# Kernel optimization log

Measured on AMD Instinct MI355X. Metric: run time of the kernel, lower is better.

The kernel has to match this reference:

```python
import jax, jax.numpy as jnp
import numpy as np

KH = KW = 3
SH = SW = 1
DH = DW = 1

def _same_padding(ih, iw):
    eff_kh = (KH - 1) * DH + 1
    eff_kw = (KW - 1) * DW + 1
    out_h = (ih + SH - 1) // SH
    out_w = (iw + SW - 1) // SW
    pad_h = max((out_h - 1) * SH + eff_kh - ih, 0)
    pad_w = max((out_w - 1) * SW + eff_kw - iw, 0)
    pad_top = pad_h // 2
    pad_bottom = pad_h - pad_top
    pad_left = pad_w // 2
    pad_right = pad_w - pad_left
    return (pad_top, pad_bottom), (pad_left, pad_right)


def setup_inputs() -> dict:
    key = jax.random.key(0)
    k1, k2, k3 = jax.random.split(key, 3)
    N, C, H, Wd = 32, 192, 56, 56
    Cout = 384
    x = jax.random.normal(k1, (N, C, H, Wd), dtype=jnp.float32)
    # linear weight (Cout, C*KH*KW) with unfold ordering (c, kh, kw) -> OIHW kernel
    W = jax.random.normal(k2, (Cout, C, KH, KW), dtype=jnp.float32) * (1.0 / np.sqrt(C * KH * KW))
    b = jax.random.normal(k3, (Cout,), dtype=jnp.float32) * 0.01
    return {"x": x, "W": W, "b": b}


def reference(x, W, b):
    # ConvLayer: F.pad('same') -> nn.Unfold -> Linear -> reshape, which is
    # mathematically a 2D conv with OIHW kernel W (unfold orders features as c,kh,kw).
    _, _, H, Wd = x.shape
    pad_hw = _same_padding(H, Wd)
    out = jax.lax.conv_general_dilated(
        x, W,
        window_strides=(SH, SW),
        padding=pad_hw,
        rhs_dilation=(DH, DW),
        dimension_numbers=("NCHW", "OIHW", "NCHW"),
    )
    return out + b[None, :, None, None]
```

## Files before the change

### kernel.cpp

```cpp
#include <hip/hip_runtime.h>
#include <cstdint>
#include <cstddef>

#define N_IMG 32
#define C_IN 192
#define HW 56
#define SPAT 3136
#define C_OUT 384
#define HP 58
#define KPOS 9
#define KTOT 1728
#define NSUB 54

#define BM 128
#define BN 256
#define NT_CO 3
#define NT_S  392
#define GRID_MAIN (NT_CO*NT_S)

typedef __attribute__((ext_vector_type(8))) short short8;
typedef __attribute__((ext_vector_type(4))) float f32x4;

__device__ __forceinline__ unsigned short f2bf(float f) {
  union { float f; unsigned u; } v; v.f = f;
  unsigned u = v.u;
  unsigned r = (u + 0x7FFFu + ((u >> 16) & 1u)) >> 16;
  return (unsigned short)r;
}

__device__ __forceinline__ void async_load16(const void* gsrc, void* ldst) {
  __builtin_amdgcn_global_load_lds(
      (const __attribute__((address_space(1))) unsigned int*)gsrc,
      (__attribute__((address_space(3))) unsigned int*)ldst,
      16, 0, 0);
}

__global__ void pack_w(const float* __restrict__ W, unsigned short* __restrict__ Wp) {
  int idx = blockIdx.x*256 + threadIdx.x;
  if (idx >= C_OUT*KPOS*C_IN) return;
  int c   = idx % C_IN;
  int pos = (idx / C_IN) % KPOS;
  int co  = idx / (C_IN*KPOS);
  float v = W[((size_t)co*C_IN + c)*KPOS + pos];
  Wp[idx] = f2bf(v);
}

__global__ void zero_border(unsigned short* __restrict__ Xp) {
  int idx = blockIdx.x*256 + threadIdx.x;
  if (idx >= N_IMG*228*C_IN) return;
  int c    = idx % C_IN;
  int cell = (idx / C_IN) % 228;
  int n    = idx / (C_IN*228);
  int hh, ww;
  if (cell < 116) { hh = (cell < 58) ? 0 : 57; ww = cell % 58; }
  else { int b2 = cell - 116; ww = (b2 < 56) ? 0 : 57; hh = 1 + (b2 % 56); }
  Xp[(((size_t)n*HP + hh)*HP + ww)*C_IN + c] = 0;
}

__global__ void pack_x(const float* __restrict__ x, unsigned short* __restrict__ Xp) {
  __shared__ float tile[64*57];
  int b  = blockIdx.x;
  int cb = b % 3;
  int h  = (b/3) % HW;
  int n  = b / (3*HW);
  int tid = threadIdx.x;
  const float* src = x + (size_t)n*C_IN*SPAT + (size_t)cb*64*SPAT + h*HW;
  #pragma unroll
  for (int i = 0; i < 14; ++i) {
    int idx = i*256 + tid;
    int c = idx / HW, w = idx % HW;
    tile[c*57 + w] = src[(size_t)c*SPAT + w];
  }
  __syncthreads();
  unsigned short* dst = Xp + (((size_t)n*HP + h + 1)*HP + 1)*C_IN + cb*64;
  #pragma unroll
  for (int i = 0; i < 14; ++i) {
    int idx = i*256 + tid;
    int w = idx / 64, c = idx % 64;
    dst[(size_t)w*C_IN + c] = f2bf(tile[c*57 + w]);
  }
}

__global__ __launch_bounds__(512, 2) void conv_gemm(
    const unsigned short* __restrict__ Wp,
    const unsigned short* __restrict__ Xp,
    const float* __restrict__ bias,
    float* __restrict__ out)
{
  __shared__ __attribute__((aligned(16))) unsigned short lds[4][12288];

  int bid = blockIdx.x;
  int wg = (bid & 7) * (GRID_MAIN/8) + (bid >> 3);
  int cotile = wg % NT_CO;
  int stile  = wg / NT_CO;

  const int tid   = threadIdx.x;
  const int lane  = tid & 63;
  const int wv    = tid >> 6;
  const int wm    = wv >> 2;
  const int wn    = wv & 3;
  const int lanep = lane & 15;
  const int laneq = lane >> 4;
  const int l2    = lane >> 2;
  const int l4    = lane & 3;
  const int chunkSw = l4 ^ (l2 & 3);

  const int aRow = cotile*BM + wv*16 + l2;
  const unsigned short* aSrc = Wp + (size_t)aRow*KTOT + chunkSw*8;

  const unsigned short* bSrc0;
  const unsigned short* bSrc1;
  {
    int r0 = (wv*2 + 0)*16 + l2;
    int f0 = stile*BN + r0;
    int n0 = f0 / SPAT, sp0 = f0 % SPAT;
    bSrc0 = Xp + (((size_t)n0*HP + sp0/HW)*HP + sp0%HW)*C_IN + chunkSw*8;
    int r1 = (wv*2 + 1)*16 + l2;
    int f1 = stile*BN + r1;
    int n1 = f1 / SPAT, sp1 = f1 % SPAT;
    bSrc1 = Xp + (((size_t)n1*HP + sp1/HW)*HP + sp1%HW)*C_IN + chunkSw*8;
  }

  unsigned short* aDst  = &lds[0][wv*512];
  unsigned short* bDst0 = &lds[0][4096 + (wv*2 + 0)*512];
  unsigned short* bDst1 = &lds[0][4096 + (wv*2 + 1)*512];

  const int swz8   = (laneq ^ (lanep & 3)) << 3;
  const int aRdBase = (wm*64 + lanep)*32 + swz8;
  const int bRdBase = 4096 + (wn*64 + lanep)*32 + swz8;

  f32x4 acc[4][4];
  #pragma unroll
  for (int mf = 0; mf < 4; ++mf)
    #pragma unroll
    for (int nf = 0; nf < 4; ++nf)
      acc[mf][nf] = (f32x4){0.f, 0.f, 0.f, 0.f};

  auto bOffOf = [](int t) {
    int kh = t / 18;
    int r  = t - kh*18;
    int kw = r / 6;
    int c6 = r - kw*6;
    return (kh*HP + kw)*C_IN + c6*32;
  };

  auto stage = [&](int t) {
    int slot = t & 3;
    async_load16(aSrc + t*32, aDst + slot*12288);
    int bo = bOffOf(t);
    async_load16(bSrc0 + bo, bDst0 + slot*12288);
    async_load16(bSrc1 + bo, bDst1 + slot*12288);
  };

#define PHASE(sv, VMC, DO_STAGE)                                            \
  {                                                                         \
    asm volatile("s_waitcnt vmcnt(" #VMC ")" ::: "memory");                 \
    __builtin_amdgcn_s_barrier();                                           \
    __builtin_amdgcn_sched_barrier(0);                                      \
    const int slot_ = (sv) & 3;                                             \
    const unsigned short* la_ = &lds[slot_][0];                             \
    short8 av_[4], bv_[4];                                                  \
    _Pragma("unroll")                                                       \
    for (int mf = 0; mf < 4; ++mf)                                          \
      av_[mf] = *(const short8*)&la_[aRdBase + mf*512];                     \
    _Pragma("unroll")                                                       \
    for (int nf = 0; nf < 4; ++nf)                                          \
      bv_[nf] = *(const short8*)&la_[bRdBase + nf*512];                     \
    if (DO_STAGE) stage((sv) + 3);                                          \
    __builtin_amdgcn_s_setprio(1);                                          \
    _Pragma("unroll")                                                       \
    for (int mf = 0; mf < 4; ++mf)                                          \
      _Pragma("unroll")                                                     \
      for (int nf = 0; nf < 4; ++nf)                                        \
        acc[mf][nf] = __builtin_amdgcn_mfma_f32_16x16x32_bf16(              \
            av_[mf], bv_[nf], acc[mf][nf], 0, 0, 0);                        \
    __builtin_amdgcn_s_setprio(0);                                          \
    __builtin_amdgcn_sched_barrier(0);                                      \
  }

  stage(0); stage(1); stage(2);

  for (int s = 0; s < 51; ++s)
    PHASE(s, 6, true);
  PHASE(51, 6, false);
  PHASE(52, 3, false);
  PHASE(53, 0, false);
#undef PHASE

  const int coB = cotile*BM + wm*64;
  const int fB  = stile*BN + wn*64;
  #pragma unroll
  for (int nf = 0; nf < 4; ++nf) {
    int f  = fB + nf*16 + lanep;
    int n  = f / SPAT;
    int sp = f % SPAT;
    float* obase = out + (size_t)n*C_OUT*SPAT + sp;
    #pragma unroll
    for (int mf = 0; mf < 4; ++mf) {
      #pragma unroll
      for (int i = 0; i < 4; ++i) {
        int co = coB + mf*16 + laneq*4 + i;
        obase[(size_t)co*SPAT] = acc[mf][nf][i] + bias[co];
      }
    }
  }
}

__global__ void conv_naive(const float* __restrict__ x, const float* __restrict__ W,
                           const float* __restrict__ bias, float* __restrict__ out) {
  size_t idx = (size_t)blockIdx.x*256 + threadIdx.x;
  if (idx >= (size_t)N_IMG*C_OUT*SPAT) return;
  int s  = idx % SPAT;
  int co = (int)((idx / SPAT) % C_OUT);
  int n  = (int)(idx / ((size_t)SPAT*C_OUT));
  int h = s / HW, w = s % HW;
  float acc = bias[co];
  for (int c = 0; c < C_IN; ++c)
    for (int kh = 0; kh < 3; ++kh) {
      int hh = h + kh - 1;
      if (hh < 0 || hh >= HW) continue;
      for (int kw = 0; kw < 3; ++kw) {
        int ww = w + kw - 1;
        if (ww < 0 || ww >= HW) continue;
        acc += x[(((size_t)n*C_IN + c)*HW + hh)*HW + ww]
             * W[(((size_t)co*C_IN + c)*3 + kh)*3 + kw];
      }
    }
  out[idx] = acc;
}

extern "C" void kernel_launch(void* const* d_in, const int* in_sizes, int n_in,
                              void* d_out, int out_size, void* d_ws, size_t ws_size,
                              hipStream_t stream) {
  const float* x = (const float*)d_in[0];
  const float* W = (const float*)d_in[1];
  const float* b = (const float*)d_in[2];
  float* out = (float*)d_out;

  const size_t WP_ELEMS = (size_t)C_OUT*KPOS*C_IN;
  const size_t XP_ELEMS = (size_t)N_IMG*HP*HP*C_IN;
  const size_t NEED = (WP_ELEMS + XP_ELEMS)*2;

  if (ws_size >= NEED) {
    unsigned short* Wp = (unsigned short*)d_ws;
    unsigned short* Xp = Wp + WP_ELEMS;
    zero_border<<<(N_IMG*228*C_IN + 255)/256, 256, 0, stream>>>(Xp);
    pack_w<<<(int)((WP_ELEMS + 255)/256), 256, 0, stream>>>(W, Wp);
    pack_x<<<N_IMG*HW*3, 256, 0, stream>>>(x, Xp);
    conv_gemm<<<GRID_MAIN, 512, 0, stream>>>(Wp, Xp, b, out);
  } else {
    size_t total = (size_t)N_IMG*C_OUT*SPAT;
    conv_naive<<<(int)((total + 255)/256), 256, 0, stream>>>(x, W, b, out);
  }
}
```

Baseline: 186.4 us.

## Double K-depth per stage with triple-buffered LDS and split barrier phases

Raises the K step per pipeline stage from 32 to 64 bf16 channels, halving the number of stages, and switches from a 4-slot ring to 3 fixed LDS buffers of 48KB each. Each stage is consumed in two MFMA half-phases with an XOR-swizzled 8-chunk layout. The barrier and vmcnt waits move to the end of each phase so LDS reads overlap with issuing the next global loads. The aim is to cut barrier and wait overhead per unit of MFMA work. The cost is more LDS per block (144KB), which may limit occupancy below the launch-bounds target of 2 blocks per CU.

Result: slower. 190.3 us (+2.1%).

```diff
diff --git a/kernel.cpp b/kernel.cpp
--- a/kernel.cpp
+++ b/kernel.cpp
@@ -10,7 +10,7 @@
 #define HP 58
 #define KPOS 9
 #define KTOT 1728
-#define NSUB 54
+#define NT 27
 
 #define BM 128
 #define BN 256
@@ -18,6 +18,9 @@
 #define NT_S  392
 #define GRID_MAIN (NT_CO*NT_S)
 
+#define BUF_EL 24576
+#define B_BASE 8192
+
 typedef __attribute__((ext_vector_type(8))) short short8;
 typedef __attribute__((ext_vector_type(4))) float f32x4;
 
@@ -34,6 +37,9 @@
       (__attribute__((address_space(3))) unsigned int*)ldst,
       16, 0, 0);
 }
+
+__device__ __forceinline__ void vm6() { asm volatile("s_waitcnt vmcnt(6)" ::: "memory"); }
+__device__ __forceinline__ void vm0() { asm volatile("s_waitcnt vmcnt(0)" ::: "memory"); }
 
 __global__ void pack_w(const float* __restrict__ W, unsigned short* __restrict__ Wp) {
   int idx = blockIdx.x*256 + threadIdx.x;
@@ -87,7 +93,7 @@
     const float* __restrict__ bias,
     float* __restrict__ out)
 {
-  __shared__ __attribute__((aligned(16))) unsigned short lds[4][12288];
+  __shared__ __attribute__((aligned(16))) unsigned short lds[3][BUF_EL];
 
   int bid = blockIdx.x;
   int wg = (bid & 7) * (GRID_MAIN/8) + (bid >> 3);
@@ -101,33 +107,37 @@
   const int wn    = wv & 3;
   const int lanep = lane & 15;
   const int laneq = lane >> 4;
-  const int l2    = lane >> 2;
-  const int l4    = lane & 3;
-  const int chunkSw = l4 ^ (l2 & 3);
-
-  const int aRow = cotile*BM + wv*16 + l2;
-  const unsigned short* aSrc = Wp + (size_t)aRow*KTOT + chunkSw*8;
-
-  const unsigned short* bSrc0;
-  const unsigned short* bSrc1;
+  const int l3    = lane >> 3;
+  const int l7    = lane & 7;
+  const int gsl   = (l7 ^ l3) << 3;
+
+  const unsigned short* aSrc0;
+  const unsigned short* aSrc1;
   {
-    int r0 = (wv*2 + 0)*16 + l2;
-    int f0 = stile*BN + r0;
-    int n0 = f0 / SPAT, sp0 = f0 % SPAT;
-    bSrc0 = Xp + (((size_t)n0*HP + sp0/HW)*HP + sp0%HW)*C_IN + chunkSw*8;
-    int r1 = (wv*2 + 1)*16 + l2;
-    int f1 = stile*BN + r1;
-    int n1 = f1 / SPAT, sp1 = f1 % SPAT;
-    bSrc1 = Xp + (((size_t)n1*HP + sp1/HW)*HP + sp1%HW)*C_IN + chunkSw*8;
-  }
-
-  unsigned short* aDst  = &lds[0][wv*512];
-  unsigned short* bDst0 = &lds[0][4096 + (wv*2 + 0)*512];
-  unsigned short* bDst1 = &lds[0][4096 + (wv*2 + 1)*512];
-
-  const int swz8   = (laneq ^ (lanep & 3)) << 3;
-  const int aRdBase = (wm*64 + lanep)*32 + swz8;
-  const int bRdBase = 4096 + (wn*64 + lanep)*32 + swz8;
+    int r0 = (0*8 + wv)*8 + l3;
+    aSrc0 = Wp + (size_t)(cotile*BM + r0)*KTOT + gsl;
+    int r1 = (1*8 + wv)*8 + l3;
+    aSrc1 = Wp + (size_t)(cotile*BM + r1)*KTOT + gsl;
+  }
+  const int aOff0 = (0*8 + wv)*512;
+  const int aOff1 = (1*8 + wv)*512;
+
+  const unsigned short* bSrc[4];
+  int bOff[4];
+  #pragma unroll
+  for (int i = 0; i < 4; ++i) {
+    int cbk = i*8 + wv;
+    int rb  = cbk*8 + l3;
+    int f   = stile*BN + rb;
+    int n   = f / SPAT, sp = f % SPAT;
+    bSrc[i] = Xp + (((size_t)n*HP + sp/HW)*HP + sp%HW)*C_IN + gsl;
+    bOff[i] = B_BASE + cbk*512;
+  }
+
+  const int swz = (laneq ^ l7) << 3;
+  const int aRd = (wm*64 + lanep)*64 + ((laneq ^ (lanep & 7)) << 3);
+  const int bRd = B_BASE + (wn*64 + lanep)*64 + ((laneq ^ (lanep & 7)) << 3);
+  (void)swz;
 
   f32x4 acc[4][4];
   #pragma unroll
@@ -137,36 +147,37 @@
       acc[mf][nf] = (f32x4){0.f, 0.f, 0.f, 0.f};
 
   auto bOffOf = [](int t) {
-    int kh = t / 18;
-    int r  = t - kh*18;
-    int kw = r / 6;
-    int c6 = r - kw*6;
-    return (kh*HP + kw)*C_IN + c6*32;
+    int pos = t / 3;
+    int c0  = (t - pos*3) * 64;
+    int kh  = pos / 3, kw = pos - kh*3;
+    return (kh*HP + kw)*C_IN + c0;
   };
 
-  auto stage = [&](int t) {
-    int slot = t & 3;
-    async_load16(aSrc + t*32, aDst + slot*12288);
-    int bo = bOffOf(t);
-    async_load16(bSrc0 + bo, bDst0 + slot*12288);
-    async_load16(bSrc1 + bo, bDst1 + slot*12288);
+  auto stage = [&](int t, unsigned short* base) {
+    const int koff = t*64;
+    async_load16(aSrc0 + koff, base + aOff0);
+    async_load16(aSrc1 + koff, base + aOff1);
+    const int bo = bOffOf(t);
+    #pragma unroll
+    for (int i = 0; i < 4; ++i)
+      async_load16(bSrc[i] + bo, base + bOff[i]);
   };
 
-#define PHASE(sv, VMC, DO_STAGE)                                            \
+#define PHASE(LB, KK, STAGE_STMT, VM_STMT)                                  \
   {                                                                         \
-    asm volatile("s_waitcnt vmcnt(" #VMC ")" ::: "memory");                 \
-    __builtin_amdgcn_s_barrier();                                           \
-    __builtin_amdgcn_sched_barrier(0);                                      \
-    const int slot_ = (sv) & 3;                                             \
-    const unsigned short* la_ = &lds[slot_][0];                             \
+    const unsigned short* lb_ = (LB);                                       \
     short8 av_[4], bv_[4];                                                  \
     _Pragma("unroll")                                                       \
     for (int mf = 0; mf < 4; ++mf)                                          \
-      av_[mf] = *(const short8*)&la_[aRdBase + mf*512];                     \
+      av_[mf] = *(const short8*)&lb_[(aRd + mf*1024) ^ ((KK)*32)];          \
     _Pragma("unroll")                                                       \
     for (int nf = 0; nf < 4; ++nf)                                          \
-      bv_[nf] = *(const short8*)&la_[bRdBase + nf*512];                     \
-    if (DO_STAGE) stage((sv) + 3);                                          \
+      bv_[nf] = *(const short8*)&lb_[(bRd + nf*1024) ^ ((KK)*32)];          \
+    STAGE_STMT;                                                             \
+    __builtin_amdgcn_sched_barrier(0);                                      \
+    __builtin_amdgcn_s_barrier();                                           \
+    asm volatile("s_waitcnt lgkmcnt(0)" ::: "memory");                      \
+    __builtin_amdgcn_sched_barrier(0);                                      \
     __builtin_amdgcn_s_setprio(1);                                          \
     _Pragma("unroll")                                                       \
     for (int mf = 0; mf < 4; ++mf)                                          \
@@ -176,15 +187,27 @@
             av_[mf], bv_[nf], acc[mf][nf], 0, 0, 0);                        \
     __builtin_amdgcn_s_setprio(0);                                          \
     __builtin_amdgcn_sched_barrier(0);                                      \
-  }
-
-  stage(0); stage(1); stage(2);
-
-  for (int s = 0; s < 51; ++s)
-    PHASE(s, 6, true);
-  PHASE(51, 6, false);
-  PHASE(52, 3, false);
-  PHASE(53, 0, false);
+    VM_STMT;                                                                \
+    __builtin_amdgcn_s_barrier();                                           \
+  }
+
+  unsigned short* b0 = &lds[0][0];
+  unsigned short* b1 = &lds[1][0];
+  unsigned short* b2 = &lds[2][0];
+
+  stage(0, b0);
+  stage(1, b1);
+  vm6();
+  __builtin_amdgcn_s_barrier();
+
+  for (int t0 = 0; t0 < NT; t0 += 3) {
+    PHASE(b0, 0, { if (t0 + 2 < NT) stage(t0 + 2, b2); }, );
+    PHASE(b0, 1, , { if (t0     < NT-2) vm6(); else vm0(); });
+    PHASE(b1, 0, { if (t0 + 3 < NT) stage(t0 + 3, b0); }, );
+    PHASE(b1, 1, , { if (t0 + 1 < NT-2) vm6(); else vm0(); });
+    PHASE(b2, 0, { if (t0 + 4 < NT) stage(t0 + 4, b1); }, );
+    PHASE(b2, 1, , { if (t0 + 2 < NT-2) vm6(); else vm0(); });
+  }
 #undef PHASE
 
   const int coB = cotile*BM + wm*64;
```
